# Performance work log

Measured on AMD Instinct MI355X. Metric: run time of the kernel, lower is better.

## Reference

```python
import jax, jax.numpy as jnp
import numpy as np

USER_NUM, ITEM_NUM = 50000, 25000
N_U, N_I = 4096, 4096
N_E, N_PRED = 262144, 65536
D, K, N_LAYERS = 64, 1000, 3
SSL_TEMP, SSL_REG, ALPHA, PROTO_REG = 0.1, 1e-6, 1.0, 8e-8


def setup_inputs() -> dict:
    key = jax.random.key(0)
    ks = jax.random.split(key, 16)
    return {
        "emb_user": jax.random.normal(ks[0], (USER_NUM, D), jnp.float32),
        "emb_item": jax.random.normal(ks[1], (ITEM_NUM, D), jnp.float32),
        "user_centroids": jax.random.normal(ks[2], (K, D), jnp.float32),
        "item_centroids": jax.random.normal(ks[3], (K, D), jnp.float32),
        "edge_u": jax.random.randint(ks[4], (N_E,), 0, N_U, jnp.int32),
        "edge_v": jax.random.randint(ks[5], (N_E,), 0, N_I, jnp.int32),
        "pos_u": jax.random.randint(ks[6], (N_PRED,), 0, N_U, jnp.int32),
        "pos_v": jax.random.randint(ks[7], (N_PRED,), 0, N_I, jnp.int32),
        "neg_u": jax.random.randint(ks[8], (N_PRED,), 0, N_U, jnp.int32),
        "neg_v": jax.random.randint(ks[9], (N_PRED,), 0, N_I, jnp.int32),
        "idx_user": jax.random.randint(ks[10], (N_U,), 0, USER_NUM, jnp.int32),
        "idx_item": jax.random.randint(ks[11], (N_I,), 0, ITEM_NUM, jnp.int32),
        "user2cluster": jax.random.randint(ks[12], (USER_NUM,), 0, K, jnp.int32),
        "item2cluster": jax.random.randint(ks[13], (ITEM_NUM,), 0, K, jnp.int32),
    }


def _l2norm(x, eps=1e-12):  # F.normalize(p=2, dim=1)
    return x / jnp.maximum(jnp.linalg.norm(x, axis=1, keepdims=True), eps)


def _ssl_loss(cur, prev, prev_total):
    nc, npv, nt = _l2norm(cur), _l2norm(prev), _l2norm(prev_total)
    pos = jnp.exp(jnp.sum(nc * npv, axis=1) / SSL_TEMP)            # [B]
    tot = jnp.exp(nc @ nt.T / SSL_TEMP).sum(axis=1)                 # [B]
    return -jnp.log(pos / tot).sum()


def _proto_loss(emb, idx, node2cluster, centroids):
    ne = _l2norm(emb)
    cents = _l2norm(centroids)                                      # run_kmeans normalizes centroids
    my_cent = cents[node2cluster[idx]]                              # [B, D]
    pos = jnp.exp(jnp.sum(ne * my_cent, axis=1) / SSL_TEMP)
    tot = jnp.exp(ne @ cents.T / SSL_TEMP).sum(axis=1)
    return -jnp.log(pos / tot).sum()


def reference(emb_user, emb_item, user_centroids, item_centroids,
              edge_u, edge_v, pos_u, pos_v, neg_u, neg_v,
              idx_user, idx_item, user2cluster, item2cluster):
    # --- symmetric-normalized bipartite GraphConv (norm='both', no weight/bias) ---
    ones_e = jnp.ones((N_E,), jnp.float32)
    deg_u = jax.ops.segment_sum(ones_e, edge_u, num_segments=N_U)
    deg_i = jax.ops.segment_sum(ones_e, edge_v, num_segments=N_I)
    inv_u = (1.0 / jnp.sqrt(jnp.maximum(deg_u, 1.0)))[:, None]      # [N_U,1]
    inv_i = (1.0 / jnp.sqrt(jnp.maximum(deg_i, 1.0)))[:, None]      # [N_I,1]

    e_u = emb_user[idx_user]                                        # initial subgraph embeddings
    e_i = emb_item[idx_item]
    res_u, res_i = e_u, e_i
    h_u, h_i = e_u, e_i
    for _ in range(N_LAYERS):
        m_u = (h_u * inv_u)[edge_u]                                 # messages along rate edges
        m_i = (h_i * inv_i)[edge_v]                                 # messages along rated-by edges
        new_i = jax.ops.segment_sum(m_u, edge_v, num_segments=N_I) * inv_i
        new_u = jax.ops.segment_sum(m_i, edge_u, num_segments=N_U) * inv_u
        h_u, h_i = new_u, new_i
        res_u = res_u + h_u
        res_i = res_i + h_i

    # --- structural-neighbour SSL loss (last layer output vs layer-0 embeddings) ---
    ssl_u = _ssl_loss(h_u, e_u, emb_user)
    ssl_i = _ssl_loss(h_i, e_i, emb_item)
    ssl_loss = SSL_REG * (ssl_u + ALPHA * ssl_i)

    # --- protoNCE loss (raw embedding-table rows vs kmeans centroids) ---
    proto_loss = PROTO_REG * (
        _proto_loss(emb_user[idx_user], idx_user, user2cluster, user_centroids)
        + _proto_loss(emb_item[idx_item], idx_item, item2cluster, item_centroids)
    )

    res_u = res_u / (N_LAYERS + 1)
    res_i = res_i / (N_LAYERS + 1)

    # --- HeteroDotProductPredictor: u_dot_v on 'rate' edges -> [E,1] ---
    pos_score = jnp.sum(res_u[pos_u] * res_i[pos_v], axis=1, keepdims=True)
    neg_score = jnp.sum(res_u[neg_u] * res_i[neg_v], axis=1, keepdims=True)
    return pos_score, neg_score, ssl_loss, proto_loss
```

## Files before the change

### kernel.cpp

```cpp
#include <hip/hip_runtime.h>
#include <hip/hip_bf16.h>

#define NU 4096
#define NI 4096
#define NE 262144
#define NPRED 65536
#define DD 64
#define KCL 1000
#define UNUM 50000
#define INUM 25000
#define NUPAD 50048
#define NIPAD 25088
#define NKPAD 1024

typedef short sh8 __attribute__((ext_vector_type(8)));
typedef float f4 __attribute__((ext_vector_type(4)));

__device__ __forceinline__ float wred64(float x){
#pragma unroll
  for(int m=1;m<64;m<<=1) x += __shfl_xor(x,m);
  return x;
}

__device__ __forceinline__ float fast_exp2(float x){
  return __builtin_amdgcn_exp2f(x);
}

__device__ __forceinline__ void gload_lds16(const void* g, void* l){
  __builtin_amdgcn_global_load_lds((const __attribute__((address_space(1))) void*)g,
                                   (__attribute__((address_space(3))) void*)l, 16, 0, 0);
}

__global__ void k_hist(const int* __restrict__ eu, const int* __restrict__ ev,
                       int* cu, int* ci){
  int t = blockIdx.x*256 + threadIdx.x;
  if(t < NE){ atomicAdd(&cu[eu[t]],1); atomicAdd(&ci[ev[t]],1); }
}

__global__ void k_scan(const int* cnt_u, int* rp_u, int* cur_u, float* inv_u,
                       const int* cnt_i, int* rp_i, int* cur_i, float* inv_i,
                       float* tot4){
  {
    int base = blockIdx.x*8192 + threadIdx.x*8;
#pragma unroll
    for(int k=0;k<8;k++) tot4[base+k] = 0.f;
  }
  const int* cnt = blockIdx.x ? cnt_i : cnt_u;
  int* rp  = blockIdx.x ? rp_i  : rp_u;
  int* cur = blockIdx.x ? cur_i : cur_u;
  float* inv = blockIdx.x ? inv_i : inv_u;
  __shared__ int sdata[1024];
  int tid = threadIdx.x;
  int v[4]; int s = 0;
#pragma unroll
  for(int k=0;k<4;k++){ v[k]=cnt[tid*4+k]; s+=v[k]; }
  sdata[tid]=s; __syncthreads();
  for(int off=1; off<1024; off<<=1){
    int add = (tid>=off)? sdata[tid-off] : 0;
    __syncthreads();
    if(tid>=off) sdata[tid] += add;
    __syncthreads();
  }
  int run = sdata[tid]-s;
#pragma unroll
  for(int k=0;k<4;k++){
    int idx = tid*4+k;
    rp[idx]=run; cur[idx]=run;
    inv[idx] = 1.0f/sqrtf(fmaxf((float)v[k],1.0f));
    run += v[k];
  }
  if(tid==1023) rp[4096]=run;
}

__global__ void k_fillgather(const int* __restrict__ eu, const int* __restrict__ ev,
                             int* cur_u, int* cur_i, int* adj_u, int* adj_i,
                             const float* __restrict__ emb_u, const float* __restrict__ emb_i,
                             const int* __restrict__ idx_u, const int* __restrict__ idx_i,
                             const float* __restrict__ inv_u, const float* __restrict__ inv_i,
                             float* e_u, float* e_i, float* res_u, float* res_i,
                             float* hs_u, float* hs_i){
  int b = blockIdx.x;
  if(b < 1024){
    int t = b*256 + threadIdx.x;
    int u=eu[t], v=ev[t];
    adj_u[atomicAdd(&cur_u[u],1)] = v;
    adj_i[atomicAdd(&cur_i[v],1)] = u;
  } else {
    int t = (b-1024)*256 + threadIdx.x;
    const int half = NU*DD;
    if(t < half){
      int r=t>>6;
      float v = emb_u[idx_u[r]*DD + (t&63)];
      e_u[t]=v; res_u[t]=v; hs_u[t]=v*inv_u[r];
    } else {
      int s=t-half; int r=s>>6;
      float v = emb_i[idx_i[r]*DD + (s&63)];
      e_i[s]=v; res_i[s]=v; hs_i[s]=v*inv_i[r];
    }
  }
}

__global__ void k_conv(const int* __restrict__ rp_i, const int* __restrict__ adj_i,
                       const float* __restrict__ hsu_in, const float* __restrict__ inv_i,
                       float* h_i, float* res_i, float* hsi_out,
                       const int* __restrict__ rp_u, const int* __restrict__ adj_u,
                       const float* __restrict__ hsi_in, const float* __restrict__ inv_u,
                       float* h_u, float* res_u, float* hsu_out){
  int b = blockIdx.x*4 + (threadIdx.x>>6);
  int lane = threadIdx.x & 63;
  const int* rp; const int* adj; const float* srcv; const float* inv;
  float *h, *res, *hso; int node;
  if(b < NI){ rp=rp_i; adj=adj_i; srcv=hsu_in; inv=inv_i; h=h_i; res=res_i; hso=hsi_out; node=b; }
  else      { node=b-NI; rp=rp_u; adj=adj_u; srcv=hsi_in; inv=inv_u; h=h_u; res=res_u; hso=hsu_out; }
  int s=rp[node], e=rp[node+1];
  float acc=0.f;
  for(int base=s; base<e; base+=64){
    int m = e-base;
    int myidx = adj[base + min(lane, m-1)];
    int kk = min(64, m);
    int k=0;
    for(; k+8<=kk; k+=8){
      int i0=__shfl(myidx,k  ), i1=__shfl(myidx,k+1),
          i2=__shfl(myidx,k+2), i3=__shfl(myidx,k+3),
          i4=__shfl(myidx,k+4), i5=__shfl(myidx,k+5),
          i6=__shfl(myidx,k+6), i7=__shfl(myidx,k+7);
      float v0=srcv[i0*DD+lane], v1=srcv[i1*DD+lane],
            v2=srcv[i2*DD+lane], v3=srcv[i3*DD+lane],
            v4=srcv[i4*DD+lane], v5=srcv[i5*DD+lane],
            v6=srcv[i6*DD+lane], v7=srcv[i7*DD+lane];
      acc += ((v0+v1)+(v2+v3)) + ((v4+v5)+(v6+v7));
    }
    for(; k<kk; k++) acc += srcv[__shfl(myidx,k)*DD+lane];
  }
  float iv = inv[node];
  float outv = acc*iv;
  h[node*DD+lane] = outv;
  res[node*DD+lane] += outv;
  hso[node*DD+lane] = outv*iv;
}

#define SB0 12512
#define SB1 (SB0+6272)
#define SB2 (SB1+256)
#define SB3 (SB2+256)
#define SB4 (SB3+1024)
#define SB5 (SB4+1024)
#define SB6 (SB5+1024)
#define SB7 (SB6+1024)

__global__ void k_normpos(const float* __restrict__ emb_u, const float* __restrict__ emb_i,
                          const float* __restrict__ ucent, const float* __restrict__ icent,
                          const float* __restrict__ h_u, const float* __restrict__ h_i,
                          const float* __restrict__ e_u, const float* __restrict__ e_i,
                          __hip_bfloat16* ntb_u, __hip_bfloat16* ntb_i,
                          __hip_bfloat16* ncb_u, __hip_bfloat16* ncb_i,
                          __hip_bfloat16* nc_u, __hip_bfloat16* nc_i,
                          __hip_bfloat16* npv_u, __hip_bfloat16* npv_i,
                          const int* __restrict__ idx_u, const int* __restrict__ idx_i,
                          const int* __restrict__ u2c, const int* __restrict__ i2c,
                          float* pos4){
  const float SC = 14.426950408889634f;
  int b = blockIdx.x;
  int lane = threadIdx.x & 63;
  if(b >= SB7){
    int w = (b-SB7)*4 + (threadIdx.x>>6);
    float hu=h_u[w*DD+lane], eu=e_u[w*DD+lane];
    float hi=h_i[w*DD+lane], ei=e_i[w*DD+lane];
    int cu = u2c[idx_u[w]], ci = i2c[idx_i[w]];
    float cuv = ucent[cu*DD+lane], civ = icent[ci*DD+lane];
    float hh = wred64(hu*hu), ee = wred64(eu*eu), he = wred64(hu*eu);
    float h2 = wred64(hi*hi), e2 = wred64(ei*ei), hei= wred64(hi*ei);
    float ccu= wred64(cuv*cuv), ecu = wred64(eu*cuv);
    float cci= wred64(civ*civ), eci = wred64(ei*civ);
    if(lane==0){
      const float eps=1e-12f;
      pos4[0*NU+w] = he  / (fmaxf(sqrtf(hh),eps)*fmaxf(sqrtf(ee),eps));
      pos4[1*NU+w] = hei / (fmaxf(sqrtf(h2),eps)*fmaxf(sqrtf(e2),eps));
      pos4[2*NU+w] = ecu / (fmaxf(sqrtf(ee),eps)*fmaxf(sqrtf(ccu),eps));
      pos4[3*NU+w] = eci / (fmaxf(sqrtf(e2),eps)*fmaxf(sqrtf(cci),eps));
    }
    return;
  }
  const float* in; __hip_bfloat16* outp; int rows; float scale; int base;
  if(b < SB0)      { in=emb_u; outp=ntb_u; rows=UNUM; scale=1.f;  base=0; }
  else if(b < SB1) { in=emb_i; outp=ntb_i; rows=INUM; scale=1.f;  base=SB0; }
  else if(b < SB2) { in=ucent; outp=ncb_u; rows=KCL;  scale=1.f;  base=SB1; }
  else if(b < SB3) { in=icent; outp=ncb_i; rows=KCL;  scale=1.f;  base=SB2; }
  else if(b < SB4) { in=h_u;   outp=nc_u;  rows=NU;   scale=SC;   base=SB3; }
  else if(b < SB5) { in=h_i;   outp=nc_i;  rows=NI;   scale=SC;   base=SB4; }
  else if(b < SB6) { in=e_u;   outp=npv_u; rows=NU;   scale=SC;   base=SB5; }
  else             { in=e_i;   outp=npv_i; rows=NI;   scale=SC;   base=SB6; }
  int row = (b-base)*4 + (threadIdx.x>>6);
  if(row >= rows){
    outp[row*DD + lane] = __float2bfloat16(0.f);
    return;
  }
  float v = in[row*DD + lane];
  float s = wred64(v*v);
  float sc = scale / fmaxf(sqrtf(s), 1e-12f);
  outp[row*DD + lane] = __float2bfloat16(v*sc);
}

#define ECH 128
#define EUU 3128
#define EUI (EUU+1568)
#define EUP0 (EUI+64)
#define EUP1 (EUP0+64)
#define EGRID 768

struct ESeg { const __hip_bfloat16* A; const __hip_bfloat16* B; float* tot; int pad; };

__global__ __launch_bounds__(256,3)
void k_expsum(ESeg s0, ESeg s1, ESeg s2, ESeg s3){
  __shared__ __hip_bfloat16 sB[2][ECH*DD];
  int tid = threadIdx.x;
  int wave = tid >> 6;
  int lane = tid & 63;
  int r = lane & 15, kq = (lane>>4)*8;

  auto resolve = [&](int u, ESeg& s, int& yc, int& x){
    int rem;
    if(u < EUU)       { s = s0; rem = u; }
    else if(u < EUI)  { s = s1; rem = u-EUU; }
    else if(u < EUP0) { s = s2; rem = u-EUI; }
    else              { s = s3; rem = u-EUP0; }
    yc = rem >> 3; x = rem & 7;
  };
  auto stage = [&](const __hip_bfloat16* B, int j_begin, int buf){
    const __hip_bfloat16* src = B + (size_t)(j_begin + wave*32 + (lane>>3))*DD + (lane&7)*8;
#pragma unroll
    for(int i=0;i<4;i++){
      gload_lds16((const void*)(src + i*8*DD), (void*)&sB[buf][(wave*32 + i*8)*DD]);
    }
  };

  { ESeg s; int yc, x; resolve(blockIdx.x, s, yc, x); stage(s.B, yc*ECH, 0); }
  int cur = 0;

  for(int u = blockIdx.x; u < EUP1; u += EGRID){
    ESeg s; int yc, x; resolve(u, s, yc, x);
    __syncthreads();
    if(u + EGRID < EUP1){
      ESeg sn; int ycn, xn; resolve(u+EGRID, sn, ycn, xn);
      stage(sn.B, ycn*ECH, cur^1);
    }
    int row0 = (x*4 + wave)*128;
    sh8 a0[8], a1[8];
#pragma unroll
    for(int t=0;t<8;t++){
      const short* ap = (const short*)(s.A + (row0 + t*16 + r)*DD);
      a0[t] = *(const sh8*)(ap + kq);
      a1[t] = *(const sh8*)(ap + kq + 32);
    }
    float acc[8][4];
#pragma unroll
    for(int t=0;t<8;t++)
#pragma unroll
      for(int q=0;q<4;q++) acc[t][q]=0.f;

    const short* sbase = (const short*)&sB[cur][0];
#pragma unroll 2
    for(int j0=0; j0<ECH; j0+=16){
      const short* bp = sbase + (j0 + r)*DD + kq;
      sh8 b0 = *(const sh8*)(bp);
      sh8 b1 = *(const sh8*)(bp + 32);
#pragma unroll
      for(int t=0;t<8;t++){
        f4 c = {0.f,0.f,0.f,0.f};
        c = __builtin_amdgcn_mfma_f32_16x16x32_bf16(a0[t], b0, c, 0,0,0);
        c = __builtin_amdgcn_mfma_f32_16x16x32_bf16(a1[t], b1, c, 0,0,0);
#pragma unroll
        for(int q=0;q<4;q++) acc[t][q] += fast_exp2(c[q]);
      }
    }
#pragma unroll
    for(int t=0;t<8;t++){
#pragma unroll
      for(int q=0;q<4;q++){
        float v = acc[t][q];
        v += __shfl_xor(v,1); v += __shfl_xor(v,2);
        v += __shfl_xor(v,4); v += __shfl_xor(v,8);
        if(r==0) atomicAdd(&s.tot[row0 + t*16 + (lane>>4)*4 + q], v);
      }
    }
    cur ^= 1;
  }
}

__global__ void k_score(const float* __restrict__ res_u, const float* __restrict__ res_i,
                        const int* __restrict__ pu, const int* __restrict__ pv,
                        const int* __restrict__ nu, const int* __restrict__ nv,
                        float* out){
  int t = blockIdx.x*256 + threadIdx.x;
  int pair = t >> 4;
  int sl = t & 15;
  if(pair >= 2*NPRED) return;
  int a,b;
  if(pair < NPRED){ a=pu[pair]; b=pv[pair]; }
  else { a=nu[pair-NPRED]; b=nv[pair-NPRED]; }
  f4 xu = *(const f4*)(res_u + a*DD + sl*4);
  f4 xv = *(const f4*)(res_i + b*DD + sl*4);
  float x = xu[0]*xv[0] + xu[1]*xv[1] + xu[2]*xv[2] + xu[3]*xv[3];
  x += __shfl_xor(x,1); x += __shfl_xor(x,2);
  x += __shfl_xor(x,4); x += __shfl_xor(x,8);
  if(sl==0) out[pair] = x*(1.0f/16.0f);
}

__global__ void k_loss(const float* __restrict__ tot4, const float* __restrict__ pos4,
                       float* out){
  const float PU_ = (float)(NUPAD-UNUM);
  const float PI_ = (float)(NIPAD-INUM);
  const float PK_ = (float)(NKPAD-KCL);
  float s0=0,s1=0,s2=0,s3=0;
  for(int b=threadIdx.x; b<NU; b+=256){
    s0 += logf(tot4[0*NU+b] - PU_) - 10.f*pos4[0*NU+b];
    s1 += logf(tot4[1*NU+b] - PI_) - 10.f*pos4[1*NU+b];
    s2 += logf(tot4[2*NU+b] - PK_) - 10.f*pos4[2*NU+b];
    s3 += logf(tot4[3*NU+b] - PK_) - 10.f*pos4[3*NU+b];
  }
  s0=wred64(s0); s1=wred64(s1); s2=wred64(s2); s3=wred64(s3);
  __shared__ float ls[4][4];
  int lane=threadIdx.x&63, w=threadIdx.x>>6;
  if(lane==0){ ls[w][0]=s0; ls[w][1]=s1; ls[w][2]=s2; ls[w][3]=s3; }
  __syncthreads();
  if(threadIdx.x==0){
    float a=0,b2=0,c=0,d=0;
#pragma unroll
    for(int k=0;k<4;k++){ a+=ls[k][0]; b2+=ls[k][1]; c+=ls[k][2]; d+=ls[k][3]; }
    out[2*NPRED]   = 1e-6f*(a+b2);
    out[2*NPRED+1] = 8e-8f*(c+d);
  }
}

extern "C" void kernel_launch(void* const* d_in, const int* in_sizes, int n_in,
                              void* d_out, int out_size, void* d_ws, size_t ws_size,
                              hipStream_t stream) {
  const float* emb_user = (const float*)d_in[0];
  const float* emb_item = (const float*)d_in[1];
  const float* ucent    = (const float*)d_in[2];
  const float* icent    = (const float*)d_in[3];
  const int* edge_u = (const int*)d_in[4];
  const int* edge_v = (const int*)d_in[5];
  const int* pos_u  = (const int*)d_in[6];
  const int* pos_v  = (const int*)d_in[7];
  const int* neg_u  = (const int*)d_in[8];
  const int* neg_v  = (const int*)d_in[9];
  const int* idx_u  = (const int*)d_in[10];
  const int* idx_i  = (const int*)d_in[11];
  const int* u2c    = (const int*)d_in[12];
  const int* i2c    = (const int*)d_in[13];
  float* out = (float*)d_out;

  char* w = (char*)d_ws;
  auto alloc = [&](size_t bytes)->void*{
    void* p = (void*)w;
    w += (bytes + 255) & ~(size_t)255;
    return p;
  };
  int* cnt_u = (int*)alloc(NU*4);
  int* cnt_i = (int*)alloc(NI*4);
  int* rp_u  = (int*)alloc((NU+1)*4);
  int* rp_i  = (int*)alloc((NI+1)*4);
  int* cur_u = (int*)alloc(NU*4);
  int* cur_i = (int*)alloc(NI*4);
  int* adj_u = (int*)alloc((size_t)NE*4);
  int* adj_i = (int*)alloc((size_t)NE*4);
  float* inv_u = (float*)alloc(NU*4);
  float* inv_i = (float*)alloc(NI*4);
  float* e_u  = (float*)alloc((size_t)NU*DD*4);
  float* e_i  = (float*)alloc((size_t)NI*DD*4);
  float* h_u  = (float*)alloc((size_t)NU*DD*4);
  float* h_i  = (float*)alloc((size_t)NI*DD*4);
  float* hsA_u = (float*)alloc((size_t)NU*DD*4);
  float* hsA_i = (float*)alloc((size_t)NI*DD*4);
  float* hsB_u = (float*)alloc((size_t)NU*DD*4);
  float* hsB_i = (float*)alloc((size_t)NI*DD*4);
  float* res_u= (float*)alloc((size_t)NU*DD*4);
  float* res_i= (float*)alloc((size_t)NI*DD*4);
  __hip_bfloat16* ntb_user = (__hip_bfloat16*)alloc((size_t)NUPAD*DD*2);
  __hip_bfloat16* ntb_item = (__hip_bfloat16*)alloc((size_t)NIPAD*DD*2);
  __hip_bfloat16* ncb_u = (__hip_bfloat16*)alloc((size_t)NKPAD*DD*2);
  __hip_bfloat16* ncb_i = (__hip_bfloat16*)alloc((size_t)NKPAD*DD*2);
  __hip_bfloat16* nc_u  = (__hip_bfloat16*)alloc((size_t)NU*DD*2);
  __hip_bfloat16* nc_i  = (__hip_bfloat16*)alloc((size_t)NI*DD*2);
  __hip_bfloat16* npv_u = (__hip_bfloat16*)alloc((size_t)NU*DD*2);
  __hip_bfloat16* npv_i = (__hip_bfloat16*)alloc((size_t)NI*DD*2);
  float* tot4 = (float*)alloc(4*NU*4);
  float* pos4 = (float*)alloc(4*NU*4);

  hipMemsetAsync(cnt_u, 0, 2*NU*4, stream);

  k_hist<<<NE/256, 256, 0, stream>>>(edge_u, edge_v, cnt_u, cnt_i);
  k_scan<<<2, 1024, 0, stream>>>(cnt_u, rp_u, cur_u, inv_u,
                                 cnt_i, rp_i, cur_i, inv_i, tot4);
  k_fillgather<<<3072, 256, 0, stream>>>(edge_u, edge_v, cur_u, cur_i, adj_u, adj_i,
                                         emb_user, emb_item, idx_u, idx_i,
                                         inv_u, inv_i,
                                         e_u, e_i, res_u, res_i, hsA_u, hsA_i);
  k_conv<<<(NU+NI)/4, 256, 0, stream>>>(rp_i, adj_i, hsA_u, inv_i, h_i, res_i, hsB_i,
                                        rp_u, adj_u, hsA_i, inv_u, h_u, res_u, hsB_u);
  k_conv<<<(NU+NI)/4, 256, 0, stream>>>(rp_i, adj_i, hsB_u, inv_i, h_i, res_i, hsA_i,
                                        rp_u, adj_u, hsB_i, inv_u, h_u, res_u, hsA_u);
  k_conv<<<(NU+NI)/4, 256, 0, stream>>>(rp_i, adj_i, hsA_u, inv_i, h_i, res_i, hsB_i,
                                        rp_u, adj_u, hsA_i, inv_u, h_u, res_u, hsB_u);

  k_normpos<<<SB7+NU/4, 256, 0, stream>>>(emb_user, emb_item, ucent, icent,
                                          h_u, h_i, e_u, e_i,
                                          ntb_user, ntb_item, ncb_u, ncb_i,
                                          nc_u, nc_i, npv_u, npv_i,
                                          idx_u, idx_i, u2c, i2c, pos4);

  ESeg su = { nc_u,  ntb_user, tot4 + 0*NU, 0 };
  ESeg si = { nc_i,  ntb_item, tot4 + 1*NU, 0 };
  ESeg sp0= { npv_u, ncb_u,    tot4 + 2*NU, 0 };
  ESeg sp1= { npv_i, ncb_i,    tot4 + 3*NU, 0 };
  k_expsum<<<EGRID, 256, 0, stream>>>(su, si, sp0, sp1);

  k_score<<<(2*NPRED*16)/256, 256, 0, stream>>>(res_u, res_i, pos_u, pos_v, neg_u, neg_v, out);
  k_loss<<<1, 256, 0, stream>>>(tot4, pos4, out);
}
```

Before: 256.1 us.

## Drop LDS double-buffering in expsum; read B directly and shrink per-wave row tile

The exp-sum GEMM kernel no longer stages B chunks into shared memory with async global-to-LDS loads and double buffering. Each wave now reads B fragments straight from global memory (L2/L1 cached), and the row tile per wave drops from 128 to 64 rows. The work-unit count is restructured accordingly and the grid and launch bounds are changed. This trades LDS traffic, sync overhead and register pressure for more redundant global loads of B and more atomics per row.

```diff
diff --git a/kernel.cpp b/kernel.cpp
--- a/kernel.cpp
+++ b/kernel.cpp
@@ -24,11 +24,6 @@
 
 __device__ __forceinline__ float fast_exp2(float x){
   return __builtin_amdgcn_exp2f(x);
-}
-
-__device__ __forceinline__ void gload_lds16(const void* g, void* l){
-  __builtin_amdgcn_global_load_lds((const __attribute__((address_space(1))) void*)g,
-                                   (__attribute__((address_space(3))) void*)l, 16, 0, 0);
 }
 
 __global__ void k_hist(const int* __restrict__ eu, const int* __restrict__ ev,
@@ -202,70 +197,51 @@
 }
 
 #define ECH 128
-#define EUU 3128
-#define EUI (EUU+1568)
-#define EUP0 (EUI+64)
-#define EUP1 (EUP0+64)
-#define EGRID 768
+#define EUU (16*391)
+#define EUI (EUU+16*196)
+#define EUP0 (EUI+16*8)
+#define EUP1 (EUP0+16*8)
+#define EGRID 2048
 
 struct ESeg { const __hip_bfloat16* A; const __hip_bfloat16* B; float* tot; int pad; };
 
-__global__ __launch_bounds__(256,3)
-void k_expsum(ESeg s0, ESeg s1, ESeg s2, ESeg s3){
-  __shared__ __hip_bfloat16 sB[2][ECH*DD];
+__global__ void k_expsum(ESeg s0, ESeg s1, ESeg s2, ESeg s3){
   int tid = threadIdx.x;
   int wave = tid >> 6;
   int lane = tid & 63;
   int r = lane & 15, kq = (lane>>4)*8;
 
-  auto resolve = [&](int u, ESeg& s, int& yc, int& x){
-    int rem;
+  for(int u = blockIdx.x; u < EUP1; u += EGRID){
+    ESeg s; int rem;
     if(u < EUU)       { s = s0; rem = u; }
     else if(u < EUI)  { s = s1; rem = u-EUU; }
     else if(u < EUP0) { s = s2; rem = u-EUI; }
     else              { s = s3; rem = u-EUP0; }
-    yc = rem >> 3; x = rem & 7;
-  };
-  auto stage = [&](const __hip_bfloat16* B, int j_begin, int buf){
-    const __hip_bfloat16* src = B + (size_t)(j_begin + wave*32 + (lane>>3))*DD + (lane&7)*8;
-#pragma unroll
-    for(int i=0;i<4;i++){
-      gload_lds16((const void*)(src + i*8*DD), (void*)&sB[buf][(wave*32 + i*8)*DD]);
-    }
-  };
-
-  { ESeg s; int yc, x; resolve(blockIdx.x, s, yc, x); stage(s.B, yc*ECH, 0); }
-  int cur = 0;
-
-  for(int u = blockIdx.x; u < EUP1; u += EGRID){
-    ESeg s; int yc, x; resolve(u, s, yc, x);
-    __syncthreads();
-    if(u + EGRID < EUP1){
-      ESeg sn; int ycn, xn; resolve(u+EGRID, sn, ycn, xn);
-      stage(sn.B, ycn*ECH, cur^1);
-    }
-    int row0 = (x*4 + wave)*128;
-    sh8 a0[8], a1[8];
-#pragma unroll
-    for(int t=0;t<8;t++){
+    int chunk = rem >> 4, x = rem & 15;
+    int row0 = x*256 + wave*64;
+    int j_begin = chunk*ECH;
+
+    sh8 a0[4], a1[4];
+#pragma unroll
+    for(int t=0;t<4;t++){
       const short* ap = (const short*)(s.A + (row0 + t*16 + r)*DD);
       a0[t] = *(const sh8*)(ap + kq);
       a1[t] = *(const sh8*)(ap + kq + 32);
     }
-    float acc[8][4];
-#pragma unroll
-    for(int t=0;t<8;t++)
+    float acc[4][4];
+#pragma unroll
+    for(int t=0;t<4;t++)
 #pragma unroll
       for(int q=0;q<4;q++) acc[t][q]=0.f;
 
-    const short* sbase = (const short*)&sB[cur][0];
+    const short* bbase = (const short*)s.B;
 #pragma unroll 2
     for(int j0=0; j0<ECH; j0+=16){
-      const short* bp = sbase + (j0 + r)*DD + kq;
+      const short* bp = bbase + (j_begin + j0 + r)*DD + kq;
       sh8 b0 = *(const sh8*)(bp);
       sh8 b1 = *(const sh8*)(bp + 32);
 #pragma unroll
-      for(int t=0;t<8;t++){
+      for(int t=0;t<4;t++){
         f4 c = {0.f,0.f,0.f,0.f};
         c = __builtin_amdgcn_mfma_f32_16x16x32_bf16(a0[t], b0, c, 0,0,0);
         c = __builtin_amdgcn_mfma_f32_16x16x32_bf16(a1[t], b1, c, 0,0,0);
@@ -274,7 +250,7 @@
       }
     }
 #pragma unroll
-    for(int t=0;t<8;t++){
+    for(int t=0;t<4;t++){
 #pragma unroll
       for(int q=0;q<4;q++){
         float v = acc[t][q];
@@ -283,7 +259,6 @@
         if(r==0) atomicAdd(&s.tot[row0 + t*16 + (lane>>4)*4 + q], v);
       }
     }
-    cur ^= 1;
   }
 }
 
```

Result: slower. 269.9 us (+5.4%).
